# Kernel optimization log

Hardware: AMD Instinct MI355X
Metric: run time of the kernel (lower is better)

## Reference

```python
import jax, jax.numpy as jnp
import numpy as np
from jax import lax

# Standard backbone geometry (angstroms / radians)
R_N_CA = 1.458
R_CA_C = 1.525
R_C_N = 1.329
A_N_CA_C = np.deg2rad(111.2)  # bond angle N-CA-C (used when placing C)
A_CA_C_N = np.deg2rad(116.2)  # bond angle CA-C-N (used when placing next N)
A_C_N_CA = np.deg2rad(121.7)  # bond angle C-N-CA (used when placing next CA)

L = 4096  # residues; num_atoms = 3*L backbone atoms (N, CA, C)


def _place_atom(A, B, C, R, theta, phi):
    """NeRF atom placement: given three previous atoms A-B-C, bond length R,
    bond angle theta (at C) and dihedral phi about B-C, return new atom D."""
    bc = C - B
    bc = bc / jnp.linalg.norm(bc)
    n = jnp.cross(B - A, bc)
    n = n / jnp.linalg.norm(n)
    m = jnp.stack([bc, jnp.cross(n, bc), n], axis=1)  # local frame, columns
    st = jnp.sin(theta)
    d2 = jnp.stack([-R * jnp.cos(theta), R * st * jnp.cos(phi), R * st * jnp.sin(phi)])
    return C + m @ d2


def _angles_to_coords(input_angles):
    # input_angles: [7, L]; rows 0,1,2 = phi, psi, omega
    phi = input_angles[0]
    psi = input_angles[1]
    omega = input_angles[2]
    dt = input_angles.dtype

    # Residue 0 placed in a canonical frame
    N0 = jnp.zeros(3, dtype=dt)
    CA0 = jnp.array([R_N_CA, 0.0, 0.0], dtype=dt)
    a = np.pi - A_N_CA_C
    C0 = CA0 + jnp.array([R_CA_C * np.cos(a), R_CA_C * np.sin(a), 0.0], dtype=dt)

    def step(carry, x):
        A, B, C = carry  # N, CA, C of previous residue
        psi_prev, om, ph = x
        Nn = _place_atom(A, B, C, R_C_N, A_CA_C_N, psi_prev)   # psi of prev residue places N
        CAn = _place_atom(B, C, Nn, R_N_CA, A_C_N_CA, om)      # omega places CA
        Cn = _place_atom(C, Nn, CAn, R_CA_C, A_N_CA_C, ph)     # phi places C
        return (Nn, CAn, Cn), jnp.stack([Nn, CAn, Cn])

    xs = (psi[:-1], omega[1:], phi[1:])
    _, rest = lax.scan(step, (N0, CA0, C0), xs)  # [L-1, 3, 3]
    first = jnp.stack([N0, CA0, C0])[None]       # [1, 3, 3]
    coords = jnp.concatenate([first, rest], axis=0)  # [L, 3, 3]
    return coords.reshape(-1)  # flat [3*num_atoms], matching the C++ op layout


def setup_inputs() -> dict:
    key = jax.random.key(0)
    u = jax.random.uniform(key, (7, L), dtype=jnp.float32)
    input_angles = u * (2.0 * np.pi) - np.pi  # dihedrals in [-pi, pi)
    return {"input_angles": input_angles}


def reference(input_angles):
    return _angles_to_coords(input_angles)
```

## Files before the change

### kernel.cpp

```cpp
#include <hip/hip_runtime.h>
#include <math.h>

namespace a2c {

constexpr float R_N_CA = 1.458f;
constexpr float R_CA_C = 1.525f;
constexpr float R_C_N  = 1.329f;
constexpr double DEG2RAD = 0.017453292519943295;
constexpr float A_NCAC = (float)(111.2 * DEG2RAD);
constexpr float A_CACN = (float)(116.2 * DEG2RAD);
constexpr float A_CNCA = (float)(121.7 * DEG2RAD);

#define A2C_MAGIC 0x5A5A17E5u

struct Xf { float r[9]; float t[3]; };

struct XfC { float c0[3]; float c1[3]; float t[3]; };

__device__ __forceinline__ Xf compose(const Xf& a, const Xf& b){
  Xf o;
#pragma unroll
  for (int i = 0; i < 3; ++i){
    o.r[3*i+0] = a.r[3*i+0]*b.r[0] + a.r[3*i+1]*b.r[3] + a.r[3*i+2]*b.r[6];
    o.r[3*i+1] = a.r[3*i+0]*b.r[1] + a.r[3*i+1]*b.r[4] + a.r[3*i+2]*b.r[7];
    o.r[3*i+2] = a.r[3*i+0]*b.r[2] + a.r[3*i+1]*b.r[5] + a.r[3*i+2]*b.r[8];
    o.t[i]     = a.r[3*i+0]*b.t[0] + a.r[3*i+1]*b.t[1] + a.r[3*i+2]*b.t[2] + a.t[i];
  }
  return o;
}

__device__ __forceinline__ XfC compose_cols(const Xf& a, const Xf& b){
  XfC o;
#pragma unroll
  for (int i = 0; i < 3; ++i){
    o.c0[i] = a.r[3*i+0]*b.r[0] + a.r[3*i+1]*b.r[3] + a.r[3*i+2]*b.r[6];
    o.c1[i] = a.r[3*i+0]*b.r[1] + a.r[3*i+1]*b.r[4] + a.r[3*i+2]*b.r[7];
    o.t[i]  = a.r[3*i+0]*b.t[0] + a.r[3*i+1]*b.t[1] + a.r[3*i+2]*b.t[2] + a.t[i];
  }
  return o;
}

__device__ __forceinline__ Xf identity_xf(){
  Xf o{};
  o.r[0] = 1.f; o.r[4] = 1.f; o.r[8] = 1.f;
  return o;
}

__device__ __forceinline__ Xf elem_full(float cT, float sT, float R, float ang){
  float sP, cP;
  __sincosf(ang, &sP, &cP);
  Xf e;
  e.r[0] = -cT;    e.r[1] = -sT;      e.r[2] = 0.f;
  e.r[3] = sT*cP;  e.r[4] = -cT*cP;   e.r[5] = -sP;
  e.r[6] = sT*sP;  e.r[7] = -cT*sP;   e.r[8] = cP;
  e.t[0] = R*e.r[0]; e.t[1] = R*e.r[3]; e.t[2] = R*e.r[6];
  return e;
}

__device__ __forceinline__ Xf compose_elemR(const Xf& a, float cT, float sT,
                                            float R, float ang){
  float sP, cP;
  __sincosf(ang, &sP, &cP);
  const float e00 = -cT,    e01 = -sT;
  const float e10 = sT*cP,  e11 = -cT*cP, e12 = -sP;
  const float e20 = sT*sP,  e21 = -cT*sP, e22 = cP;
  Xf o;
#pragma unroll
  for (int i = 0; i < 3; ++i){
    const float a0 = a.r[3*i+0], a1 = a.r[3*i+1], a2 = a.r[3*i+2];
    o.r[3*i+0] = a0*e00 + a1*e10 + a2*e20;
    o.r[3*i+1] = a0*e01 + a1*e11 + a2*e21;
    o.r[3*i+2] =          a1*e12 + a2*e22;
    o.t[i]     = R*o.r[3*i+0] + a.t[i];
  }
  return o;
}

__device__ __forceinline__ Xf step_closed(float ps, float om, float ph){
  const float cCACN = cosf(A_CACN), sCACN = sinf(A_CACN);
  const float cCNCA = cosf(A_CNCA), sCNCA = sinf(A_CNCA);
  const float cNCAC = cosf(A_NCAC), sNCAC = sinf(A_NCAC);
  Xf e = elem_full(cCACN, sCACN, R_C_N, ps);
  e = compose_elemR(e, cCNCA, sCNCA, R_N_CA, om);
  e = compose_elemR(e, cNCAC, sNCAC, R_CA_C, ph);
  return e;
}

__device__ __forceinline__ Xf append_step(const Xf& a, float ps, float om, float ph){
  const float cCACN = cosf(A_CACN), sCACN = sinf(A_CACN);
  const float cCNCA = cosf(A_CNCA), sCNCA = sinf(A_CNCA);
  const float cNCAC = cosf(A_NCAC), sNCAC = sinf(A_NCAC);
  Xf o = compose_elemR(a, cCACN, sCACN, R_C_N,  ps);
  o = compose_elemR(o, cCNCA, sCNCA, R_N_CA, om);
  o = compose_elemR(o, cNCAC, sNCAC, R_CA_C, ph);
  return o;
}

__device__ __forceinline__ Xf g0_xf(){
  const float cNCAC = cosf(A_NCAC), sNCAC = sinf(A_NCAC);
  const float ca = -cNCAC, sa = sNCAC;
  Xf g;
  g.r[0]=ca;  g.r[1]=-sa; g.r[2]=0.f;
  g.r[3]=sa;  g.r[4]=ca;  g.r[5]=0.f;
  g.r[6]=0.f; g.r[7]=0.f; g.r[8]=1.f;
  g.t[0]=R_N_CA + R_CA_C*ca;
  g.t[1]=R_CA_C*sa;
  g.t[2]=0.f;
  return g;
}

__device__ __forceinline__ void emit_c(float* __restrict__ out, int k, const XfC& G){
  const float cNCAC = cosf(A_NCAC), sNCAC = sinf(A_NCAC);
  const float ax = -R_CA_C + R_N_CA*cNCAC;
  const float ay = R_N_CA*sNCAC;
  const float bx = -R_CA_C;
  float* o = out + 9*k;
  o[0] = ax*G.c0[0] + ay*G.c1[0] + G.t[0];
  o[1] = ax*G.c0[1] + ay*G.c1[1] + G.t[1];
  o[2] = ax*G.c0[2] + ay*G.c1[2] + G.t[2];
  o[3] = bx*G.c0[0] + G.t[0];
  o[4] = bx*G.c0[1] + G.t[1];
  o[5] = bx*G.c0[2] + G.t[2];
  o[6] = G.t[0]; o[7] = G.t[1]; o[8] = G.t[2];
}

__device__ __forceinline__ void emit(float* __restrict__ out, int k, const Xf& G){
  XfC c;
#pragma unroll
  for (int i = 0; i < 3; ++i){
    c.c0[i] = G.r[3*i+0]; c.c1[i] = G.r[3*i+1]; c.t[i] = G.t[i];
  }
  emit_c(out, k, c);
}

__device__ __forceinline__ Xf shfl_up_xf(const Xf& x, int d){
  Xf o;
  const float* s = (const float*)&x;
  float* p = (float*)&o;
#pragma unroll
  for (int i = 0; i < 12; ++i) p[i] = __shfl_up(s[i], d, 64);
  return o;
}

__global__ __launch_bounds__(512)
void lookback_kernel(const float* __restrict__ ang, float* __restrict__ out,
                     float* __restrict__ ws, int Lr){
  __shared__ Xf s_inc[8];
  __shared__ Xf s_pre;
  __shared__ Xf s_tot[8];
  const int b = blockIdx.x;
  const int NB = gridDim.x;
  const int t = threadIdx.x;
  const int lane = t & 63;
  const int wv = t >> 6;
  const int k = b*512 + t;
  const float* phi = ang;
  const float* psi = ang + Lr;
  const float* omg = ang + 2*Lr;
  unsigned* flags = (unsigned*)ws + 256;

  Xf Mi;
  if (k == 0)      Mi = g0_xf();
  else if (k < Lr) Mi = step_closed(psi[k-1], omg[k], phi[k]);
  else             Mi = identity_xf();

  Xf inc = Mi;
#pragma unroll
  for (int d = 1; d < 64; d <<= 1){
    Xf up = shfl_up_xf(inc, d);
    if (lane >= d) inc = compose(up, inc);
  }
  if (lane == 63) s_tot[wv] = inc;
  __syncthreads();

  if (t < 8){
    Xf w = s_tot[t];
#pragma unroll
    for (int d = 1; d < 8; d <<= 1){
      Xf up = shfl_up_xf(w, d);
      if (lane >= d) w = compose(up, w);
    }
    s_inc[t] = w;
    if (t == 7 && NB > 1){
      float* dst = ws + 16*b;
      const float* sv = (const float*)&w;
#pragma unroll
      for (int i = 0; i < 12; ++i) dst[i] = sv[i];
      __threadfence();
      __hip_atomic_store(&flags[b], A2C_MAGIC, __ATOMIC_RELEASE,
                         __HIP_MEMORY_SCOPE_AGENT);
    }
  }
  if (t == 0){
    Xf pre = identity_xf();
    for (int j = 0; j < b; ++j){
      while (__hip_atomic_load(&flags[j], __ATOMIC_ACQUIRE,
                               __HIP_MEMORY_SCOPE_AGENT) != A2C_MAGIC){}
      Xf Tj;
      const float* src = ws + 16*j;
      float* dv = (float*)&Tj;
#pragma unroll
      for (int i = 0; i < 12; ++i) dv[i] = src[i];
      pre = (j == 0) ? Tj : compose(pre, Tj);
    }
    s_pre = pre;
  }
  __syncthreads();

  Xf pre = s_pre;
  if (wv > 0) pre = compose(pre, s_inc[wv-1]);
  Xf laneExcl = shfl_up_xf(inc, 1);
  if (lane > 0) pre = compose(pre, laneExcl);
  if (k < Lr){
    XfC G = compose_cols(pre, Mi);
    emit_c(out, k, G);
  }
}

template<int CHUNK>
__global__ __launch_bounds__(1024)
void fused1024_kernel(const float* __restrict__ ang, float* __restrict__ out, int Lr){
  __shared__ Xf s_tot[64];
  __shared__ Xf s_inc[16];
  const int t = threadIdx.x;
  const int lane = t & 63;
  const int wv = t >> 6;
  const int k0 = t * CHUNK;
  const float* phi = ang;
  const float* psi = ang + Lr;
  const float* omg = ang + 2*Lr;

  Xf Mi[CHUNK];
  {
    const int k = k0;
    if (k == 0)      Mi[0] = g0_xf();
    else if (k < Lr) Mi[0] = step_closed(psi[k-1], omg[k], phi[k]);
    else             Mi[0] = identity_xf();
  }
#pragma unroll
  for (int j = 1; j < CHUNK; ++j){
    const int k = k0 + j;
    if (k < Lr) Mi[j] = append_step(Mi[j-1], psi[k-1], omg[k], phi[k]);
    else        Mi[j] = Mi[j-1];
  }

  Xf inc = Mi[CHUNK-1];
#pragma unroll
  for (int d = 1; d < 64; d <<= 1){
    Xf up = shfl_up_xf(inc, d);
    if (lane >= d) inc = compose(up, inc);
  }

  if (t >= 16 && t < 64) s_tot[t] = identity_xf();
  if (lane == 63) s_tot[wv] = inc;
  __syncthreads();

  if (t < 64){
    Xf w = s_tot[t];
#pragma unroll
    for (int d = 1; d < 16; d <<= 1){
      Xf up = shfl_up_xf(w, d);
      if (lane >= d) w = compose(up, w);
    }
    if (t < 16) s_inc[t] = w;
  }
  __syncthreads();

  Xf laneExcl = shfl_up_xf(inc, 1);
  Xf pre;
  if (wv == 0) pre = (lane == 0) ? identity_xf() : laneExcl;
  else         pre = (lane == 0) ? s_inc[wv-1] : compose(s_inc[wv-1], laneExcl);

#pragma unroll
  for (int j = 0; j < CHUNK; ++j){
    const int k = k0 + j;
    if (k < Lr){
      XfC G = compose_cols(pre, Mi[j]);
      emit_c(out, k, G);
    }
  }
}

__global__ __launch_bounds__(256)
void scan_fallback_kernel(const float* __restrict__ ang, float* __restrict__ out, int Lr){
  __shared__ Xf s[256];
  const int t = threadIdx.x;
  const int chunk = (Lr + 255) >> 8;
  const int k0 = t * chunk;
  const int k1 = (k0 + chunk < Lr) ? (k0 + chunk) : Lr;
  const float* phi = ang;
  const float* psi = ang + Lr;
  const float* omg = ang + 2*Lr;

  Xf P = identity_xf();
  for (int k = k0; k < k1; ++k){
    Xf T = (k == 0) ? g0_xf() : step_closed(psi[k-1], omg[k], phi[k]);
    P = (k == k0) ? T : compose(P, T);
  }
  s[t] = P;
  __syncthreads();

  Xf cur = P;
  for (int d = 1; d < 256; d <<= 1){
    Xf left;
    const bool has = (t >= d);
    if (has) left = s[t - d];
    __syncthreads();
    if (has){ cur = compose(left, cur); s[t] = cur; }
    __syncthreads();
  }

  Xf G = (t == 0) ? identity_xf() : s[t - 1];
  for (int k = k0; k < k1; ++k){
    G = (k == 0) ? compose(G, g0_xf())
                 : append_step(G, psi[k-1], omg[k], phi[k]);
    emit(out, k, G);
  }
}

}

extern "C" void kernel_launch(void* const* d_in, const int* in_sizes, int n_in,
                              void* d_out, int out_size, void* d_ws, size_t ws_size,
                              hipStream_t stream){
  const float* ang = (const float*)d_in[0];
  float* out = (float*)d_out;
  const int Lr = in_sizes[0] / 7;
  (void)n_in; (void)out_size;
  const bool ws_ok = (ws_size >= 4096);
  if (Lr <= 8*512 && ws_ok){
    const int NB = (Lr + 511) / 512;
    hipLaunchKernelGGL(a2c::lookback_kernel, dim3(NB), dim3(512), 0, stream,
                       ang, out, (float*)d_ws, Lr);
  } else if (Lr <= 1024*8){
    hipLaunchKernelGGL((a2c::fused1024_kernel<8>), dim3(1), dim3(1024), 0, stream,
                       ang, out, Lr);
  } else if (Lr <= 1024*16){
    hipLaunchKernelGGL((a2c::fused1024_kernel<16>), dim3(1), dim3(1024), 0, stream,
                       ang, out, Lr);
  } else {
    hipLaunchKernelGGL(a2c::scan_fallback_kernel, dim3(1), dim3(256), 0, stream,
                       ang, out, Lr);
  }
}
```

Before: 14.65 us.

## Parallelize lookback prefix gather and stage block output through LDS for coalesced stores

In the decoupled-lookback kernel, the serial single-thread loop over predecessor block totals is replaced by up to 8 lanes each waiting on one flag, followed by a shuffle-down tree reduction that composes the transforms. Each block's 9-float-per-residue outputs are also staged in shared memory and written back as coalesced float4 stores instead of strided 36-byte per-thread writes. This costs an extra 18 KB of LDS and one more barrier. The tree reduction only covers 8 predecessors, so with more than 9 blocks the prefix would be incomplete, which is fine for L=4096 with 512-thread blocks.

```diff
diff --git a/kernel.cpp b/kernel.cpp
--- a/kernel.cpp
+++ b/kernel.cpp
@@ -109,12 +109,11 @@
   return g;
 }
 
-__device__ __forceinline__ void emit_c(float* __restrict__ out, int k, const XfC& G){
+__device__ __forceinline__ void coords9(const XfC& G, float* __restrict__ o){
   const float cNCAC = cosf(A_NCAC), sNCAC = sinf(A_NCAC);
   const float ax = -R_CA_C + R_N_CA*cNCAC;
   const float ay = R_N_CA*sNCAC;
   const float bx = -R_CA_C;
-  float* o = out + 9*k;
   o[0] = ax*G.c0[0] + ay*G.c1[0] + G.t[0];
   o[1] = ax*G.c0[1] + ay*G.c1[1] + G.t[1];
   o[2] = ax*G.c0[2] + ay*G.c1[2] + G.t[2];
@@ -130,7 +129,7 @@
   for (int i = 0; i < 3; ++i){
     c.c0[i] = G.r[3*i+0]; c.c1[i] = G.r[3*i+1]; c.t[i] = G.t[i];
   }
-  emit_c(out, k, c);
+  coords9(c, out + 9*k);
 }
 
 __device__ __forceinline__ Xf shfl_up_xf(const Xf& x, int d){
@@ -139,6 +138,15 @@
   float* p = (float*)&o;
 #pragma unroll
   for (int i = 0; i < 12; ++i) p[i] = __shfl_up(s[i], d, 64);
+  return o;
+}
+
+__device__ __forceinline__ Xf shfl_down_xf(const Xf& x, int d){
+  Xf o;
+  const float* s = (const float*)&x;
+  float* p = (float*)&o;
+#pragma unroll
+  for (int i = 0; i < 12; ++i) p[i] = __shfl_down(s[i], d, 64);
   return o;
 }
 
@@ -148,6 +156,7 @@
   __shared__ Xf s_inc[8];
   __shared__ Xf s_pre;
   __shared__ Xf s_tot[8];
+  __shared__ float s_out[512*9];
   const int b = blockIdx.x;
   const int NB = gridDim.x;
   const int t = threadIdx.x;
@@ -190,20 +199,21 @@
       __hip_atomic_store(&flags[b], A2C_MAGIC, __ATOMIC_RELEASE,
                          __HIP_MEMORY_SCOPE_AGENT);
     }
-  }
-  if (t == 0){
-    Xf pre = identity_xf();
-    for (int j = 0; j < b; ++j){
-      while (__hip_atomic_load(&flags[j], __ATOMIC_ACQUIRE,
+    Xf V = identity_xf();
+    if (t < b){
+      while (__hip_atomic_load(&flags[t], __ATOMIC_ACQUIRE,
                                __HIP_MEMORY_SCOPE_AGENT) != A2C_MAGIC){}
-      Xf Tj;
-      const float* src = ws + 16*j;
-      float* dv = (float*)&Tj;
+      const float* src = ws + 16*t;
+      float* dv = (float*)&V;
 #pragma unroll
       for (int i = 0; i < 12; ++i) dv[i] = src[i];
-      pre = (j == 0) ? Tj : compose(pre, Tj);
-    }
-    s_pre = pre;
+    }
+#pragma unroll
+    for (int dd = 1; dd < 8; dd <<= 1){
+      Xf dn = shfl_down_xf(V, dd);
+      if ((t & (2*dd - 1)) == 0) V = compose(V, dn);
+    }
+    if (t == 0) s_pre = V;
   }
   __syncthreads();
 
@@ -211,9 +221,28 @@
   if (wv > 0) pre = compose(pre, s_inc[wv-1]);
   Xf laneExcl = shfl_up_xf(inc, 1);
   if (lane > 0) pre = compose(pre, laneExcl);
-  if (k < Lr){
+  {
     XfC G = compose_cols(pre, Mi);
-    emit_c(out, k, G);
+    float o9[9];
+    coords9(G, o9);
+#pragma unroll
+    for (int i = 0; i < 9; ++i) s_out[9*t + i] = o9[i];
+  }
+  __syncthreads();
+
+  const int rem = Lr - b*512;
+  if (rem >= 512){
+    const float4* src4 = (const float4*)s_out;
+    float4* dst4 = (float4*)(out + (size_t)b*512*9);
+#pragma unroll
+    for (int i = 0; i < 9; ++i){
+      const int idx = t + 512*i;
+      if (idx < 1152) dst4[idx] = src4[idx];
+    }
+  } else if (rem > 0){
+    const int F = rem*9;
+    float* dst = out + (size_t)b*512*9;
+    for (int i = t; i < F; i += 512) dst[i] = s_out[i];
   }
 }
 
@@ -276,7 +305,11 @@
     const int k = k0 + j;
     if (k < Lr){
       XfC G = compose_cols(pre, Mi[j]);
-      emit_c(out, k, G);
+      float o9[9];
+      coords9(G, o9);
+      float* o = out + 9*k;
+#pragma unroll
+      for (int i = 0; i < 9; ++i) o[i] = o9[i];
     }
   }
 }
```

After: 12.75 us. 1.15x faster.
